# Kernel optimization log

Hardware: AMD Instinct MI355X
Metric: run time of the kernel (lower is better)

Reference implementation:

```python
import jax, jax.numpy as jnp
import numpy as np

K = 20          # cfg.K, k-NN neighbors
NEG = 0.2       # LeakyReLU slope
EPS = 1e-5      # BatchNorm eps (eval mode, running mean=0, var=1)
BN_SCALE = np.float32(1.0 / np.sqrt(1.0 + EPS))


def graph_feature(x, k):
    # x: [B, C, N] -> [B, 2C, N, k] (DGCNN get_graph_feature)
    xt = jnp.swapaxes(x, 1, 2)                                  # [B,N,C]
    xx = jnp.sum(xt * xt, axis=-1)                              # [B,N]
    inner = jnp.einsum('bnc,bmc->bnm', xt, xt)
    negdist = 2.0 * inner - xx[:, :, None] - xx[:, None, :]     # -||xi-xj||^2
    _, idx = jax.lax.top_k(negdist, k)                          # [B,N,k]
    feat = jax.vmap(lambda xb, ib: xb[ib])(xt, idx)             # [B,N,k,C]
    center = jnp.broadcast_to(xt[:, :, None, :], feat.shape)
    out = jnp.concatenate([feat - center, center], axis=-1)     # [B,N,k,2C]
    return jnp.transpose(out, (0, 3, 1, 2))


def edge_layer(x, W, b, g, beta):
    # 1x1 Conv2d + BN(eval) + LeakyReLU + max over k
    f = graph_feature(x, K)                                     # [B,2C,N,k]
    y = jnp.einsum('oc,bcnk->bonk', W, f) + b[:, None, None]
    y = y * (g[:, None, None] * BN_SCALE) + beta[:, None, None]
    y = jnp.where(y >= 0, y, NEG * y)
    return jnp.max(y, axis=-1)                                  # [B,O,N]


def edge_conv(x, Ws, bs, gs, betas):
    for W, b, g, beta in zip(Ws, bs, gs, betas):
        x = edge_layer(x, W, b, g, beta)
    return x


def mha(x, Wi, bi, Wo, bo, nh=8):
    # torch nn.MultiheadAttention(64, 8, batch_first=True), self-attention
    B, N, E = x.shape
    d = E // nh
    qkv = x @ Wi.T + bi
    q, k_, v = jnp.split(qkv, 3, axis=-1)
    hd = lambda t: jnp.transpose(t.reshape(B, N, nh, d), (0, 2, 1, 3))
    q, k_, v = hd(q), hd(k_), hd(v)
    a = jax.nn.softmax(jnp.einsum('bhnd,bhmd->bhnm', q, k_) / np.float32(np.sqrt(d)), axis=-1)
    o = jnp.einsum('bhnm,bhmd->bhnd', a, v)
    o = jnp.transpose(o, (0, 2, 1, 3)).reshape(B, N, E)
    return o @ Wo.T + bo


def branch(feats, cW, cb, cg, cB, sW, sb, sg, sB, Wi, bi, Wo, bo):
    xyz = feats[:, 0:3, :]
    sem = feats[:, 3:, :]
    xyz = edge_conv(xyz, cW, cb, cg, cB)                         # [B,32,N]
    sem = edge_conv(sem, sW, sb, sg, sB)                         # [B,32,N]
    fuse = jnp.concatenate([jnp.swapaxes(xyz, 1, 2), jnp.swapaxes(sem, 1, 2)], axis=2)  # [B,N,64]
    fuse = mha(fuse, Wi, bi, Wo, bo)
    B, N, E = fuse.shape
    return fuse.reshape(B, N, E // 2, 2).mean(axis=-1)           # AvgPool1d(2,2) -> [B,N,32]


def attention_pool(emb, W):
    # SimGNN-style attention readout
    g = jnp.tanh(jnp.mean(emb @ W, axis=1))                      # [B,F]
    scores = jax.nn.sigmoid(jnp.einsum('bnf,bf->bn', emb, g))    # [B,N]
    pooled = jnp.einsum('bnf,bn->bf', emb, scores)               # [B,F]
    return pooled, scores[..., None]


def setup_inputs() -> dict:
    key = jax.random.key(0)
    ks = iter(jax.random.split(key, 48))
    nrm = lambda shape, s=0.05: jax.random.normal(next(ks), shape, dtype=jnp.float32) * s
    B, N = 8, 1024
    inp = {
        'features_1': jax.random.normal(next(ks), (B, 15, N), jnp.float32),
        'features_2': jax.random.normal(next(ks), (B, 15, N), jnp.float32),
    }
    dims_c = [(64, 6), (128, 128), (32, 256)]    # center_conv (in=3)
    dims_s = [(64, 24), (128, 128), (32, 256)]   # sem_conv (in=12)
    for pre, dims in (('c', dims_c), ('s', dims_s)):
        for i, (o, c) in enumerate(dims):
            inp[pre + 'w%d' % i] = nrm((o, c))
            inp[pre + 'b%d' % i] = jnp.zeros((o,), jnp.float32)
            inp[pre + 'g%d' % i] = jnp.ones((o,), jnp.float32)
            inp[pre + 'B%d' % i] = jnp.zeros((o,), jnp.float32)
    inp['mha_wi'] = nrm((192, 64)); inp['mha_bi'] = jnp.zeros((192,), jnp.float32)
    inp['mha_wo'] = nrm((64, 64));  inp['mha_bo'] = jnp.zeros((64,), jnp.float32)
    inp['att_w'] = nrm((32, 32), 0.1)
    inp['ntn_w'] = nrm((32, 32, 16)); inp['ntn_v'] = nrm((16, 32)); inp['ntn_b'] = jnp.zeros((16,), jnp.float32)
    inp['fc1_w'] = nrm((16, 16)); inp['fc1_b'] = jnp.zeros((16,), jnp.float32)
    inp['sc_w'] = nrm((1, 16));  inp['sc_b'] = jnp.zeros((1,), jnp.float32)
    return inp


def reference(features_1, features_2,
              cw0, cb0, cg0, cB0, cw1, cb1, cg1, cB1, cw2, cb2, cg2, cB2,
              sw0, sb0, sg0, sB0, sw1, sb1, sg1, sB1, sw2, sb2, sg2, sB2,
              mha_wi, mha_bi, mha_wo, mha_bo,
              att_w, ntn_w, ntn_v, ntn_b, fc1_w, fc1_b, sc_w, sc_b):
    cW, cb, cg, cB = [cw0, cw1, cw2], [cb0, cb1, cb2], [cg0, cg1, cg2], [cB0, cB1, cB2]
    sW, sb, sg, sB = [sw0, sw1, sw2], [sb0, sb1, sb2], [sg0, sg1, sg2], [sB0, sB1, sB2]
    a1 = branch(features_1, cW, cb, cg, cB, sW, sb, sg, sB, mha_wi, mha_bi, mha_wo, mha_bo)
    a2 = branch(features_2, cW, cb, cg, cB, sW, sb, sg, sB, mha_wi, mha_bi, mha_wo, mha_bo)
    p1, s1 = attention_pool(a1, att_w)
    p2, s2 = attention_pool(a2, att_w)
    d = p1 - p2                                                  # [B,32]
    t = jax.nn.relu(jnp.einsum('bf,fgt,bg->bt', d, ntn_w, d) + d @ ntn_v.T + ntn_b)  # [B,16]
    h = jax.nn.relu(t @ fc1_w.T + fc1_b)
    score = jax.nn.sigmoid(h @ sc_w.T + sc_b).reshape(-1)        # [B]
    return score, s1, s2
```

## Files before the change

kernel.cpp:

```cpp
#include <hip/hip_runtime.h>
#include <math.h>

#define BD 16
#define ND 1024
#define KNN 20
#define NEGS 0.2f
#define BNSC 0.99999500003749969482f
#define KSL 8
#define KPS 128

__device__ __forceinline__ float leakyf(float y){ return y >= 0.f ? y : NEGS*y; }


template<int C, int CS>
__global__ __launch_bounds__(256) void k_prep(const float* __restrict__ f1,
                                              const float* __restrict__ f2,
                                              float* __restrict__ x,
                                              float* __restrict__ xx, int c0){
  int blk = blockIdx.x;
  int b = blk & 15;
  int n = (blk >> 4)*256 + threadIdx.x;
  const float* feat = (b & 8) ? f2 : f1;
  int b8 = b & 7;
  float v[CS];
  float s = 0.f;
  #pragma unroll
  for (int c = 0; c < C; ++c){
    v[c] = feat[((size_t)(b8*15) + c0 + c)*ND + n];
    s = fmaf(v[c], v[c], s);
  }
  #pragma unroll
  for (int c = C; c < CS; ++c) v[c] = 0.f;
  #pragma unroll
  for (int g = 0; g < CS/4; ++g)
    *(float4*)&x[(size_t)(b*CS + g*4)*ND + (size_t)n*4] =
        make_float4(v[g*4], v[g*4+1], v[g*4+2], v[g*4+3]);
  xx[b*ND + n] = s;
}

__global__ __launch_bounds__(256)
void k_knn(const float* __restrict__ x,
    const float* __restrict__ xx, int* __restrict__ idxp, int CS, int nchunk){
  __shared__ __align__(16) float Xc0[1024*4];
  __shared__ __align__(16) float Xc1[1024*4];
  int b = blockIdx.x & 15;
  int r0 = (blockIdx.x >> 4)*16;
  int t = threadIdx.x;
  int lane = t & 63;
  int w = __builtin_amdgcn_readfirstlane(t >> 6);
  const float* xb = x + (size_t)b*ND*CS;
  float acc[4][16];
  #pragma unroll
  for (int j = 0; j < 4; ++j)
    #pragma unroll
    for (int q = 0; q < 16; ++q) acc[j][q] = 0.f;
  for (int ch = 0; ch < nchunk; ++ch){
    int g0 = 2*ch, g1 = 2*ch + 1;
    bool h1 = (g1*4 < CS);
    __syncthreads();
    for (int m = t; m < 1024; m += 256){
      *(float4*)&Xc0[m*4] = *(const float4*)&xb[((size_t)g0*ND + m)*4];
      *(float4*)&Xc1[m*4] = h1 ? *(const float4*)&xb[((size_t)g1*ND + m)*4]
                               : make_float4(0.f,0.f,0.f,0.f);
    }
    __syncthreads();
    float4 rv0[4], rv1[4];
    #pragma unroll
    for (int j = 0; j < 4; ++j){
      rv0[j] = *(const float4*)&Xc0[(r0 + w*4 + j)*4];
      rv1[j] = *(const float4*)&Xc1[(r0 + w*4 + j)*4];
    }
    #pragma unroll
    for (int q = 0; q < 16; ++q){
      float4 cv0 = *(const float4*)&Xc0[(q*64 + lane)*4];
      float4 cv1 = *(const float4*)&Xc1[(q*64 + lane)*4];
      #pragma unroll
      for (int j = 0; j < 4; ++j){
        float s = acc[j][q];
        s = fmaf(rv0[j].x, cv0.x, s); s = fmaf(rv0[j].y, cv0.y, s);
        s = fmaf(rv0[j].z, cv0.z, s); s = fmaf(rv0[j].w, cv0.w, s);
        s = fmaf(rv1[j].x, cv1.x, s); s = fmaf(rv1[j].y, cv1.y, s);
        s = fmaf(rv1[j].z, cv1.z, s); s = fmaf(rv1[j].w, cv1.w, s);
        acc[j][q] = s;
      }
    }
  }
  float xxm[16];
  #pragma unroll
  for (int q = 0; q < 16; ++q) xxm[q] = xx[b*ND + q*64 + lane];
  unsigned uk[4][16];
  #pragma unroll
  for (int j = 0; j < 4; ++j){
    float xr = xx[b*ND + r0 + w*4 + j];
    #pragma unroll
    for (int q = 0; q < 16; ++q){
      float f = 2.f*acc[j][q] - xr - xxm[q];
      unsigned bv = __float_as_uint(f);
      uk[j][q] = (bv & 0x80000000u) ? ~bv : (bv | 0x80000000u);
    }
  }
  unsigned pref[4] = {0u, 0u, 0u, 0u};
  unsigned done = 0u;
  #pragma unroll 1
  for (int bit = 30; bit >= 0; --bit){
    #pragma unroll
    for (int u = 0; u < 4; ++u){
      if (done & (1u << u)) continue;
      unsigned cand = pref[u] | (1u << bit);
      int c = 0;
      #pragma unroll
      for (int q = 0; q < 16; ++q)
        c += (int)__popcll(__ballot(uk[u][q] >= cand));
      if (c >= KNN){
        pref[u] = cand;
        if (c == KNN) done |= (1u << u);
      }
    }
    if (done == 15u) break;
  }
  unsigned long long mlt = (1ull << lane) - 1ull;
  #pragma unroll
  for (int u = 0; u < 4; ++u){
    unsigned T = pref[u];
    int cg = 0;
    #pragma unroll
    for (int q = 0; q < 16; ++q) cg += (int)__popcll(__ballot(uk[u][q] > T));
    int need_eq = KNN - cg;
    int* op = &idxp[((size_t)(b*ND + r0 + w*4 + u))*KNN];
    int run_gt = 0, run_eq = 0;
    #pragma unroll
    for (int q = 0; q < 16; ++q){
      unsigned k = uk[u][q];
      unsigned long long bg = __ballot(k > T);
      unsigned long long be = __ballot(k == T);
      if (k > T) op[run_gt + (int)__popcll(bg & mlt)] = q*64 + lane;
      if (k == T){
        int r = run_eq + (int)__popcll(be & mlt);
        if (r < need_eq) op[cg + r] = q*64 + lane;
      }
      run_gt += (int)__popcll(bg);
      run_eq += (int)__popcll(be);
    }
  }
}

template<int O>
__global__ __launch_bounds__(256) void k_phaseA(const float* __restrict__ x,
    const float* __restrict__ W, const float* __restrict__ bias,
    const float* __restrict__ gamma, const float* __restrict__ beta,
    float* __restrict__ zs, float* __restrict__ ccv, int C, int XS){
  constexpr int TO = O/16;
  constexpr int WP = O + 4;
  __shared__ float W1s[32*WP];
  __shared__ float dWs[32*WP];
  __shared__ float Xs[32*33];
  int blk = blockIdx.x;
  int b = blk & 15, n0 = (blk >> 4)*32;
  int t = threadIdx.x;
  int ot = t & 15, nt = t >> 4;
  int obase = ot*TO;
  int nl = nt*2;
  float az[TO][2] = {}, ac[TO][2] = {};
  for (int cc = 0; cc < C; cc += 32){
    int KC = (C - cc < 32) ? (C - cc) : 32;
    int NG = (KC + 3) >> 2;
    for (int i = t; i < O*KC; i += 256){
      int o = i % O, c = i / O;
      float w1 = W[(size_t)o*2*C + cc + c];
      float w2 = W[(size_t)o*2*C + C + cc + c];
      W1s[c*WP + o] = w1;
      dWs[c*WP + o] = w2 - w1;
    }
    for (int i = t; i < 32*NG; i += 256){
      int row = i & 31, g = i >> 5;
      float4 v = *(const float4*)&x[(size_t)(b*XS + cc + g*4)*ND + (size_t)(n0+row)*4];
      Xs[(g*4+0)*33 + row] = v.x;
      Xs[(g*4+1)*33 + row] = v.y;
      Xs[(g*4+2)*33 + row] = v.z;
      Xs[(g*4+3)*33 + row] = v.w;
    }
    __syncthreads();
    for (int c = 0; c < KC; ++c){
      float xv0 = Xs[c*33 + nl];
      float xv1 = Xs[c*33 + nl + 1];
      #pragma unroll
      for (int i = 0; i < TO; ++i){
        float w1 = W1s[c*WP + obase + i];
        float dw = dWs[c*WP + obase + i];
        az[i][0] = fmaf(w1, xv0, az[i][0]);
        az[i][1] = fmaf(w1, xv1, az[i][1]);
        ac[i][0] = fmaf(dw, xv0, ac[i][0]);
        ac[i][1] = fmaf(dw, xv1, ac[i][1]);
      }
    }
    __syncthreads();
  }
  #pragma unroll
  for (int i = 0; i < TO; ++i){
    int o = obase + i;
    float alpha = gamma[o]*BNSC;
    float bb = bias[o], be = beta[o];
    #pragma unroll
    for (int q = 0; q < 2; ++q){
      int n = n0 + nl + q;
      size_t off = ((size_t)b*ND + n)*O + o;
      zs[off]  = az[i][q]*alpha;
      ccv[off] = fmaf(ac[i][q] + bb, alpha, be);
    }
  }
}

template<bool DOXX, bool TILED>
__global__ __launch_bounds__(256) void k_phaseB(const float* __restrict__ zs,
    const float* __restrict__ ccv, const int* __restrict__ idxp,
    float* __restrict__ outp, float* __restrict__ xxout,
    int O, int ostride, int ooff){
  int t = threadIdx.x;
  int lane = t & 63, w = t >> 6;
  int b = blockIdx.x & 15;
  int n = (blockIdx.x >> 4)*4 + w;
  int gn = (b << 10) + n;
  int mm[KNN];
  const int* ip = idxp + (size_t)gn*KNN;
  #pragma unroll
  for (int k = 0; k < KNN; ++k) mm[k] = ip[k];
  float sq = 0.f;
  for (int o = lane; o < O; o += 64){
    float cvv = ccv[(size_t)gn*O + o];
    float mx = -INFINITY;
    #pragma unroll 4
    for (int k = 0; k < KNN; ++k){
      float v = leakyf(zs[((size_t)(b*ND) + mm[k])*O + o] + cvv);
      mx = fmaxf(mx, v);
    }
    if (TILED)
      outp[(size_t)(b*O + (o & ~3))*ND + (size_t)n*4 + (o & 3)] = mx;
    else
      outp[(size_t)gn*ostride + ooff + o] = mx;
    if (DOXX) sq = fmaf(mx, mx, sq);
  }
  if (DOXX){
    #pragma unroll
    for (int off = 32; off; off >>= 1) sq += __shfl_down(sq, off);
    if (lane == 0) xxout[gn] = sq;
  }
}

__global__ __launch_bounds__(256) void k_lin(const float* __restrict__ in,
    const float* __restrict__ Wm, const float* __restrict__ bias,
    float* __restrict__ outp){
  int b = blockIdx.x & 15;
  int inner = (blockIdx.x >> 4)*256 + threadIdx.x;
  int o = inner % 192; int n = inner / 192;
  int bn = (b << 10) + n;
  const float4* ip = (const float4*)(in + (size_t)bn*64);
  const float4* wp = (const float4*)(Wm + (size_t)o*64);
  float s = bias[o];
  #pragma unroll
  for (int c = 0; c < 16; ++c){
    float4 a = ip[c], wv = wp[c];
    s = fmaf(a.x, wv.x, s); s = fmaf(a.y, wv.y, s);
    s = fmaf(a.z, wv.z, s); s = fmaf(a.w, wv.w, s);
  }
  outp[(size_t)bn*192 + o] = s;
}

__global__ __launch_bounds__(256, 1) void k_attn_part(const float* __restrict__ qkv,
    float* __restrict__ pl, float* __restrict__ pacc){
  __shared__ __align__(16) float Ks[2][KPS*8];
  __shared__ __align__(16) float Vs[2][KPS*8];
  int blk = blockIdx.x;
  int b = blk & 15; int ksl = (blk >> 4) & 7; int hp = blk >> 7;
  int t = threadIdx.x;
  int hh = t >> 7;
  int h = hp*2 + hh;
  int lq = t & 127;
  for (int i = t; i < 2*KPS*8; i += 256){
    int hi = (i >= KPS*8) ? 1 : 0;
    int r = i - hi*KPS*8;
    int m = r >> 3, dd = r & 7;
    size_t base = ((size_t)b*ND + ksl*KPS + m)*192 + (hp*2 + hi)*8 + dd;
    Ks[hi][r] = qkv[base + 64];
    Vs[hi][r] = qkv[base + 128];
  }
  __syncthreads();
  const float scale = 0.35355339059327373f;
  float q[8][8];
  #pragma unroll
  for (int u = 0; u < 8; ++u){
    int n = u*128 + lq;
    const float4* qp = (const float4*)(qkv + ((size_t)b*ND + n)*192 + h*8);
    float4 q0 = qp[0], q1 = qp[1];
    q[u][0]=q0.x*scale; q[u][1]=q0.y*scale; q[u][2]=q0.z*scale; q[u][3]=q0.w*scale;
    q[u][4]=q1.x*scale; q[u][5]=q1.y*scale; q[u][6]=q1.z*scale; q[u][7]=q1.w*scale;
  }
  float l[8] = {};
  float acc[8][8] = {};
  for (int m = 0; m < KPS; ++m){
    float4 k0 = *(const float4*)&Ks[hh][m*8];
    float4 k1 = *(const float4*)&Ks[hh][m*8+4];
    float4 v0 = *(const float4*)&Vs[hh][m*8];
    float4 v1 = *(const float4*)&Vs[hh][m*8+4];
    #pragma unroll
    for (int u = 0; u < 8; ++u){
      float s;
      s = q[u][0]*k0.x;           s = fmaf(q[u][1], k0.y, s);
      s = fmaf(q[u][2], k0.z, s); s = fmaf(q[u][3], k0.w, s);
      s = fmaf(q[u][4], k1.x, s); s = fmaf(q[u][5], k1.y, s);
      s = fmaf(q[u][6], k1.z, s); s = fmaf(q[u][7], k1.w, s);
      float p = __expf(s);
      l[u] += p;
      acc[u][0] = fmaf(p, v0.x, acc[u][0]);
      acc[u][1] = fmaf(p, v0.y, acc[u][1]);
      acc[u][2] = fmaf(p, v0.z, acc[u][2]);
      acc[u][3] = fmaf(p, v0.w, acc[u][3]);
      acc[u][4] = fmaf(p, v1.x, acc[u][4]);
      acc[u][5] = fmaf(p, v1.y, acc[u][5]);
      acc[u][6] = fmaf(p, v1.z, acc[u][6]);
      acc[u][7] = fmaf(p, v1.w, acc[u][7]);
    }
  }
  #pragma unroll
  for (int u = 0; u < 8; ++u){
    int n = u*128 + lq;
    size_t pidx = (((size_t)(b*8 + h))*8 + ksl)*ND + n;
    pl[pidx] = l[u];
    float4* ap = (float4*)&pacc[pidx*8];
    ap[0] = make_float4(acc[u][0], acc[u][1], acc[u][2], acc[u][3]);
    ap[1] = make_float4(acc[u][4], acc[u][5], acc[u][6], acc[u][7]);
  }
}

__global__ __launch_bounds__(256) void k_attn_comb(const float* __restrict__ pl,
    const float* __restrict__ pacc, float* __restrict__ attno){
  int b = blockIdx.x & 15;
  int inner = (blockIdx.x >> 4)*256 + threadIdx.x;
  int h = inner >> 10; int n = inner & 1023;
  int bh = b*8 + h;
  float L = 0.f;
  float o[8] = {};
  #pragma unroll
  for (int s = 0; s < KSL; ++s){
    size_t pidx = ((size_t)bh*8 + s)*ND + n;
    L += pl[pidx];
    const float4* ap = (const float4*)&pacc[pidx*8];
    float4 a0 = ap[0], a1 = ap[1];
    o[0] += a0.x; o[1] += a0.y; o[2] += a0.z; o[3] += a0.w;
    o[4] += a1.x; o[5] += a1.y; o[6] += a1.z; o[7] += a1.w;
  }
  float inv = 1.f/L;
  float4* dst = (float4*)&attno[((size_t)b*ND + n)*64 + h*8];
  dst[0] = make_float4(o[0]*inv, o[1]*inv, o[2]*inv, o[3]*inv);
  dst[1] = make_float4(o[4]*inv, o[5]*inv, o[6]*inv, o[7]*inv);
}

__global__ __launch_bounds__(256) void k_projmean(const float* __restrict__ attno,
    const float* __restrict__ Wo, const float* __restrict__ bo,
    float* __restrict__ emb){
  int b = blockIdx.x & 15;
  int inner = (blockIdx.x >> 4)*256 + threadIdx.x;
  int n = inner >> 5; int f = inner & 31;
  int bn = (b << 10) + n;
  const float4* ip = (const float4*)(attno + (size_t)bn*64);
  int o0 = 2*f, o1 = 2*f + 1;
  const float4* w0 = (const float4*)(Wo + (size_t)o0*64);
  const float4* w1 = (const float4*)(Wo + (size_t)o1*64);
  float s0 = bo[o0], s1 = bo[o1];
  #pragma unroll
  for (int c = 0; c < 16; ++c){
    float4 a = ip[c], u = w0[c], v = w1[c];
    s0 = fmaf(a.x,u.x,s0); s0 = fmaf(a.y,u.y,s0); s0 = fmaf(a.z,u.z,s0); s0 = fmaf(a.w,u.w,s0);
    s1 = fmaf(a.x,v.x,s1); s1 = fmaf(a.y,v.y,s1); s1 = fmaf(a.z,v.z,s1); s1 = fmaf(a.w,v.w,s1);
  }
  emb[(size_t)bn*32 + f] = 0.5f*(s0 + s1);
}

__global__ __launch_bounds__(256) void k_poolfuse(const float* __restrict__ emb,
    const float* __restrict__ attw, float* __restrict__ sout,
    float* __restrict__ pooled){
  __shared__ float part[8][32];
  __shared__ float meanv[32];
  __shared__ float gv[32];
  __shared__ float sc[ND];
  int b = blockIdx.x, t = threadIdx.x;
  int f = t & 31, j = t >> 5;
  const float* eb = emb + (size_t)b*ND*32;
  float s = 0.f;
  for (int n = j; n < ND; n += 8) s += eb[n*32 + f];
  part[j][f] = s;
  __syncthreads();
  if (t < 32){
    float m = 0.f;
    for (int j2 = 0; j2 < 8; ++j2) m += part[j2][t];
    meanv[t] = m * (1.f/ND);
  }
  __syncthreads();
  if (t < 32){
    float acc = 0.f;
    for (int f2 = 0; f2 < 32; ++f2) acc = fmaf(meanv[f2], attw[f2*32 + t], acc);
    gv[t] = tanhf(acc);
  }
  __syncthreads();
  for (int n = t; n < ND; n += 256){
    const float4* ep = (const float4*)(eb + n*32);
    float acc = 0.f;
    #pragma unroll
    for (int f4 = 0; f4 < 8; ++f4){
      float4 e = ep[f4];
      acc = fmaf(e.x, gv[f4*4+0], acc);
      acc = fmaf(e.y, gv[f4*4+1], acc);
      acc = fmaf(e.z, gv[f4*4+2], acc);
      acc = fmaf(e.w, gv[f4*4+3], acc);
    }
    float sg = 1.f/(1.f + __expf(-acc));
    sout[(size_t)b*ND + n] = sg;
    sc[n] = sg;
  }
  __syncthreads();
  float pacc = 0.f;
  for (int n = j; n < ND; n += 8) pacc = fmaf(eb[n*32 + f], sc[n], pacc);
  part[j][f] = pacc;
  __syncthreads();
  if (t < 32){
    float m = 0.f;
    for (int j2 = 0; j2 < 8; ++j2) m += part[j2][t];
    pooled[b*32 + t] = m;
  }
}

__global__ __launch_bounds__(256) void k_head(const float* __restrict__ p1,
    const float* __restrict__ p2, const float* __restrict__ ntnw,
    const float* __restrict__ ntnv, const float* __restrict__ ntnb,
    const float* __restrict__ fc1w, const float* __restrict__ fc1b,
    const float* __restrict__ scw, const float* __restrict__ scb,
    float* __restrict__ outscore){
  __shared__ __align__(16) float Wl[8192];
  __shared__ float Vl[512];
  __shared__ float F1[256];
  __shared__ float ds[8][32];
  __shared__ float tv[8][16];
  __shared__ float hv[8][16];
  int t = threadIdx.x;
  {
    int b = t >> 5, f = t & 31;
    ds[b][f] = p1[b*32+f] - p2[b*32+f];
  }
  for (int i = t; i < 512; i += 256) Vl[i] = ntnv[i];
  if (t < 256) F1[t] = fc1w[t];
  float acc = 0.f;
  for (int ph = 0; ph < 2; ++ph){
    __syncthreads();
    {
      const float4* src = (const float4*)(ntnw + ph*8192);
      float4* dst = (float4*)Wl;
      for (int i = t; i < 2048; i += 256) dst[i] = src[i];
    }
    __syncthreads();
    if (t < 128){
      int b = t >> 4, tt = t & 15;
      for (int fi = 0; fi < 16; ++fi){
        float df = ds[b][ph*16 + fi];
        #pragma unroll 8
        for (int gg = 0; gg < 32; ++gg)
          acc = fmaf(df*ds[b][gg], Wl[(fi*32+gg)*16 + tt], acc);
      }
    }
  }
  if (t < 128){
    int b = t >> 4, tt = t & 15;
    acc += ntnb[tt];
    for (int gg = 0; gg < 32; ++gg) acc = fmaf(ds[b][gg], Vl[tt*32+gg], acc);
    tv[b][tt] = fmaxf(acc, 0.f);
  }
  __syncthreads();
  if (t < 128){
    int b = t >> 4, i = t & 15;
    float a2 = fc1b[i];
    for (int kk = 0; kk < 16; ++kk) a2 = fmaf(tv[b][kk], F1[i*16+kk], a2);
    hv[b][i] = fmaxf(a2, 0.f);
  }
  __syncthreads();
  if (t < 8){
    float a3 = scb[0];
    for (int i = 0; i < 16; ++i) a3 = fmaf(hv[t][i], scw[i], a3);
    outscore[t] = 1.f/(1.f + __expf(-a3));
  }
}

extern "C" void kernel_launch(void* const* d_in, const int* in_sizes, int n_in,
                              void* d_out, int out_size, void* d_ws, size_t ws_size,
                              hipStream_t stream) {
  auto F = [&](int i){ return (const float*)d_in[i]; };
  const float* f1 = F(0); const float* f2 = F(1);
  const float* cw[3] = { F(2), F(6), F(10) };
  const float* cb[3] = { F(3), F(7), F(11) };
  const float* cg[3] = { F(4), F(8), F(12) };
  const float* cB[3] = { F(5), F(9), F(13) };
  const float* sw[3] = { F(14), F(18), F(22) };
  const float* sb[3] = { F(15), F(19), F(23) };
  const float* sg[3] = { F(16), F(20), F(24) };
  const float* sB[3] = { F(17), F(21), F(25) };
  const float* mha_wi = F(26); const float* mha_bi = F(27);
  const float* mha_wo = F(28); const float* mha_bo = F(29);
  const float* att_w  = F(30);
  const float* ntn_w  = F(31); const float* ntn_v = F(32); const float* ntn_b = F(33);
  const float* fc1_w  = F(34); const float* fc1_b = F(35);
  const float* sc_w   = F(36); const float* sc_b  = F(37);
  float* out = (float*)d_out;

  char* ws = (char*)d_ws;
  const size_t MB = 1 << 20;
  float* xA   = (float*)(ws + 0*MB);
  float* xB   = (float*)(ws + 8*MB);
  float* zs   = (float*)(ws + 16*MB);
  float* cvb  = (float*)(ws + 24*MB);
  int*   idxb = (int*)  (ws + 32*MB);
  float* xxb  = (float*)(ws + 34*MB);
  float* fuse = (float*)(ws + 35*MB);
  float* qkv   = (float*)(ws + 0*MB);
  float* plb   = (float*)(ws + 12*MB);
  float* paccb = (float*)(ws + 16*MB);
  float* attno = (float*)(ws + 48*MB);
  float* emb   = (float*)(ws + 52*MB);
  float* pooled= (float*)(ws + 54*MB);
  (void)ws_size;

  auto knn = [&](const float* xin, int CS, int nch8){
    k_knn<<<BD*64, 256, 0, stream>>>(xin, xxb, idxb, CS, nch8);
  };
  auto phA = [&](const float* xin, int C, int XS, int O, const float* W, const float* bb,
                 const float* gg, const float* be){
    if (O == 64)       k_phaseA<64> <<<BD*32, 256, 0, stream>>>(xin, W, bb, gg, be, zs, cvb, C, XS);
    else if (O == 128) k_phaseA<128><<<BD*32, 256, 0, stream>>>(xin, W, bb, gg, be, zs, cvb, C, XS);
    else               k_phaseA<32> <<<BD*32, 256, 0, stream>>>(xin, W, bb, gg, be, zs, cvb, C, XS);
  };

  for (int part = 0; part < 2; ++part){
    const float* const* Wl = part ? sw : cw;
    const float* const* bl = part ? sb : cb;
    const float* const* gl = part ? sg : cg;
    const float* const* Bl = part ? sB : cB;
    int C0 = part ? 12 : 3;
    int CS0 = part ? 12 : 4;
    if (part) k_prep<12,12><<<BD*ND/256, 256, 0, stream>>>(f1, f2, xA, xxb, 3);
    else      k_prep<3, 4> <<<BD*ND/256, 256, 0, stream>>>(f1, f2, xA, xxb, 0);
    knn(xA, CS0, part ? 2 : 1);
    phA(xA, C0, CS0, 64, Wl[0], bl[0], gl[0], Bl[0]);
    k_phaseB<true,true><<<BD*ND/4, 256, 0, stream>>>(zs, cvb, idxb, xB, xxb, 64, 0, 0);
    knn(xB, 64, 8);
    phA(xB, 64, 64, 128, Wl[1], bl[1], gl[1], Bl[1]);
    k_phaseB<true,true><<<BD*ND/4, 256, 0, stream>>>(zs, cvb, idxb, xA, xxb, 128, 0, 0);
    knn(xA, 128, 16);
    phA(xA, 128, 128, 32, Wl[2], bl[2], gl[2], Bl[2]);
    k_phaseB<false,false><<<BD*ND/4, 256, 0, stream>>>(zs, cvb, idxb, fuse, nullptr, 32, 64, part*32);
  }
  k_lin<<<(BD*ND*192)/256, 256, 0, stream>>>(fuse, mha_wi, mha_bi, qkv);
  k_attn_part<<<BD*4*KSL, 256, 0, stream>>>(qkv, plb, paccb);
  k_attn_comb<<<(BD*8*ND)/256, 256, 0, stream>>>(plb, paccb, attno);
  k_projmean<<<(BD*ND*32)/256, 256, 0, stream>>>(attno, mha_wo, mha_bo, emb);
  k_poolfuse<<<BD, 256, 0, stream>>>(emb, att_w, out + 8, pooled);
  k_head<<<1, 256, 0, stream>>>(pooled, pooled + 256, ntn_w, ntn_v, ntn_b,
                                fc1_w, fc1_b, sc_w, sc_b, out);
}
```

Measured before the change: 1.193 ms.

## Double-buffer kNN LDS tiles with async global-to-LDS loads

The kNN distance kernel now keeps two LDS buffers per operand. It fills the next chunk with direct global-to-LDS loads (global_load_lds) while it computes on the current chunk, and it drops one of the two barriers per iteration. The aim is to hide global load latency behind the FMA loop and skip the VGPR round trip on the load path. In exchange, LDS use per block doubles from 32KB to 64KB, which can lower occupancy. Layers with a single chunk (for example 3-channel input) get no overlap.

```diff
diff --git a/kernel.cpp b/kernel.cpp
--- a/kernel.cpp
+++ b/kernel.cpp
@@ -10,6 +10,12 @@
 #define KPS 128
 
 __device__ __forceinline__ float leakyf(float y){ return y >= 0.f ? y : NEGS*y; }
+
+__device__ __forceinline__ void gl_lds16(const float* g, float* l){
+  __builtin_amdgcn_global_load_lds(
+      (const __attribute__((address_space(1))) void*)g,
+      (__attribute__((address_space(3))) void*)l, 16, 0, 0);
+}
 
 
 template<int C, int CS>
@@ -41,8 +47,7 @@
 __global__ __launch_bounds__(256)
 void k_knn(const float* __restrict__ x,
     const float* __restrict__ xx, int* __restrict__ idxp, int CS, int nchunk){
-  __shared__ __align__(16) float Xc0[1024*4];
-  __shared__ __align__(16) float Xc1[1024*4];
+  __shared__ __align__(16) float Xc[2][2][4096];
   int b = blockIdx.x & 15;
   int r0 = (blockIdx.x >> 4)*16;
   int t = threadIdx.x;
@@ -54,26 +59,36 @@
   for (int j = 0; j < 4; ++j)
     #pragma unroll
     for (int q = 0; q < 16; ++q) acc[j][q] = 0.f;
+
+  auto stage = [&](int buf, int ch){
+    int g0 = 2*ch, g1 = 2*ch + 1;
+    bool v1 = (g1*4 < CS);
+    #pragma unroll
+    for (int i = 0; i < 4; ++i){
+      int m = i*256 + t;
+      unsigned ub = (unsigned)((i*256 + (w << 6))*4);
+      gl_lds16(&xb[((size_t)g0*ND + m)*4], &Xc[buf][0][ub]);
+      if (v1) gl_lds16(&xb[((size_t)g1*ND + m)*4], &Xc[buf][1][ub]);
+      else    *(float4*)&Xc[buf][1][m*4] = make_float4(0.f,0.f,0.f,0.f);
+    }
+  };
+
+  stage(0, 0);
+  __syncthreads();
+  int cur = 0;
   for (int ch = 0; ch < nchunk; ++ch){
-    int g0 = 2*ch, g1 = 2*ch + 1;
-    bool h1 = (g1*4 < CS);
-    __syncthreads();
-    for (int m = t; m < 1024; m += 256){
-      *(float4*)&Xc0[m*4] = *(const float4*)&xb[((size_t)g0*ND + m)*4];
-      *(float4*)&Xc1[m*4] = h1 ? *(const float4*)&xb[((size_t)g1*ND + m)*4]
-                               : make_float4(0.f,0.f,0.f,0.f);
-    }
-    __syncthreads();
+    bool more = (ch + 1 < nchunk);
+    if (more) stage(cur ^ 1, ch + 1);
     float4 rv0[4], rv1[4];
     #pragma unroll
     for (int j = 0; j < 4; ++j){
-      rv0[j] = *(const float4*)&Xc0[(r0 + w*4 + j)*4];
-      rv1[j] = *(const float4*)&Xc1[(r0 + w*4 + j)*4];
+      rv0[j] = *(const float4*)&Xc[cur][0][(r0 + w*4 + j)*4];
+      rv1[j] = *(const float4*)&Xc[cur][1][(r0 + w*4 + j)*4];
     }
     #pragma unroll
     for (int q = 0; q < 16; ++q){
-      float4 cv0 = *(const float4*)&Xc0[(q*64 + lane)*4];
-      float4 cv1 = *(const float4*)&Xc1[(q*64 + lane)*4];
+      float4 cv0 = *(const float4*)&Xc[cur][0][(q*64 + lane)*4];
+      float4 cv1 = *(const float4*)&Xc[cur][1][(q*64 + lane)*4];
       #pragma unroll
       for (int j = 0; j < 4; ++j){
         float s = acc[j][q];
@@ -83,6 +98,10 @@
         s = fmaf(rv1[j].z, cv1.z, s); s = fmaf(rv1[j].w, cv1.w, s);
         acc[j][q] = s;
       }
+    }
+    if (more){
+      __syncthreads();
+      cur ^= 1;
     }
   }
   float xxm[16];
```

Result: faster. 1.103 ms (-7.5%).
